# Kernel optimization log

Measured on AMD Instinct MI355X. Metric: run time of the kernel, lower is better.

The kernel has to match this reference:

```python
import jax, jax.numpy as jnp
import numpy as np

N_HEADS = 16
W_INIT_SCALE = 0.02  # GPT-2 style init so activations stay well-conditioned


def setup_inputs() -> dict:
    key = jax.random.key(0)
    k1, k2, k3 = jax.random.split(key, 3)
    B, S, H = 2, 2048, 2048
    return {
        "hidden_states": jax.random.normal(k1, (B, S, H), dtype=jnp.float32),
        "w_attn": jax.random.normal(k2, (H, 3 * H), dtype=jnp.float32) * W_INIT_SCALE,
        "b_attn": jnp.zeros((3 * H,), dtype=jnp.float32),
        "w_proj": jax.random.normal(k3, (H, H), dtype=jnp.float32) * W_INIT_SCALE,
        "b_proj": jnp.zeros((H,), dtype=jnp.float32),
    }


def reference(hidden_states, w_attn, b_attn, w_proj, b_proj):
    B, S, H = hidden_states.shape
    d = H // N_HEADS
    scale = d ** -0.5

    # c_attn: packed QKV projection, then chunk along last dim
    qkv = hidden_states @ w_attn + b_attn  # [B, S, 3H]
    q, k, v = jnp.split(qkv, 3, axis=-1)
    q = q.reshape(B, S, N_HEADS, d)
    k = k.reshape(B, S, N_HEADS, d)
    v = v.reshape(B, S, N_HEADS, d)

    # causal multi-head attention (prompt-phase path of GPTCacheFlowAttention)
    scores = jnp.einsum("bqhd,bkhd->bhqk", q, k) * scale  # [B, H, S, S]
    causal = jnp.tril(jnp.ones((S, S), dtype=bool))
    scores = jnp.where(causal, scores, jnp.finfo(scores.dtype).min)
    probs = jax.nn.softmax(scores, axis=-1)
    attn = jnp.einsum("bhqk,bkhd->bqhd", probs, v).reshape(B, S, H)

    # c_proj output projection
    return attn @ w_proj + b_proj
```

## Files before the change

### kernel.cpp

```cpp
#include <hip/hip_runtime.h>
#include <hip/hip_bf16.h>
#include <stdint.h>

typedef __hip_bfloat16 bf16;
typedef __attribute__((ext_vector_type(4))) float f32x4;
typedef __attribute__((ext_vector_type(8))) short short8;

#define DEVI static __device__ __forceinline__
#define SM_SCALE 0.08838834764831845f

DEVI void gload_lds16(const bf16* g, bf16* l) {
  __builtin_amdgcn_global_load_lds(
      (const __attribute__((address_space(1))) unsigned int*)g,
      (__attribute__((address_space(3))) unsigned int*)l, 16, 0, 0);
}

__global__ __launch_bounds__(256) void cvt_f32_bf16(const float* __restrict__ in,
                                                    bf16* __restrict__ out, int n8) {
  int i = blockIdx.x * blockDim.x + threadIdx.x;
  if (i >= n8) return;
  const float4 a = *(const float4*)(in + (size_t)i * 8);
  const float4 b = *(const float4*)(in + (size_t)i * 8 + 4);
  bf16 t[8];
  t[0] = __float2bfloat16(a.x); t[1] = __float2bfloat16(a.y);
  t[2] = __float2bfloat16(a.z); t[3] = __float2bfloat16(a.w);
  t[4] = __float2bfloat16(b.x); t[5] = __float2bfloat16(b.y);
  t[6] = __float2bfloat16(b.z); t[7] = __float2bfloat16(b.w);
  *(short8*)(out + (size_t)i * 8) = *(const short8*)t;
}

__global__ __launch_bounds__(256) void transpose_cvt(const float* __restrict__ in,
                                                     bf16* __restrict__ out,
                                                     int R, int C, int scale_lt,
                                                     float scale) {
  __shared__ bf16 tile[64][72];
  const int c0 = blockIdx.x * 64, r0 = blockIdx.y * 64;
  const int t = threadIdx.x;
#pragma unroll
  for (int i = 0; i < 4; i++) {
    int idx = (i * 256 + t) * 4;
    int r = idx >> 6, c = idx & 63;
    float4 v = *(const float4*)&in[(size_t)(r0 + r) * C + c0 + c];
    float s0 = (c0 + c + 0 < scale_lt) ? scale : 1.f;
    float s1 = (c0 + c + 1 < scale_lt) ? scale : 1.f;
    float s2 = (c0 + c + 2 < scale_lt) ? scale : 1.f;
    float s3 = (c0 + c + 3 < scale_lt) ? scale : 1.f;
    tile[c + 0][r] = __float2bfloat16(v.x * s0);
    tile[c + 1][r] = __float2bfloat16(v.y * s1);
    tile[c + 2][r] = __float2bfloat16(v.z * s2);
    tile[c + 3][r] = __float2bfloat16(v.w * s3);
  }
  __syncthreads();
#pragma unroll
  for (int i = 0; i < 2; i++) {
    int idx = (i * 256 + t) * 8;
    int c = idx >> 6, r = idx & 63;
    *(short8*)&out[(size_t)(c0 + c) * R + r0 + r] = *(const short8*)&tile[c][r];
  }
}

__global__ __launch_bounds__(256) void build_vt(const bf16* __restrict__ qkv,
                                                bf16* __restrict__ vt) {
  __shared__ bf16 tile[64][72];
  const int bh = blockIdx.z, b = bh >> 4, h = bh & 15;
  const bf16* src = qkv + (size_t)b * 2048 * 6144 + 4096 + (size_t)h * 128;
  bf16* dst = vt + (size_t)bh * 128 * 2048;
  const int s0 = blockIdx.y * 64, d0 = blockIdx.x * 64;
  const int t = threadIdx.x;
#pragma unroll
  for (int i = 0; i < 2; i++) {
    int idx = (i * 256 + t) * 8;
    int r = idx >> 6, c = idx & 63;
    short8 v = *(const short8*)&src[(size_t)(s0 + r) * 6144 + d0 + c];
    bf16* vv = (bf16*)&v;
#pragma unroll
    for (int j = 0; j < 8; j++) tile[c + j][r] = vv[j];
  }
  __syncthreads();
#pragma unroll
  for (int i = 0; i < 2; i++) {
    int idx = (i * 256 + t) * 8;
    int r = idx >> 6, c = idx & 63;
    *(short8*)&dst[(size_t)(d0 + r) * 2048 + s0 + c] = *(const short8*)&tile[r][c];
  }
}

template <int OUT_BF16>
__global__ __launch_bounds__(256, 2) void gemm_bt(const bf16* __restrict__ A,
                                                  const bf16* __restrict__ Bt,
                                                  const float* __restrict__ bias,
                                                  void* __restrict__ C,
                                                  const int M, const int N, const int K,
                                                  const int bias_lt, const float bscale) {
  __shared__ bf16 As[128 * 32];
  __shared__ bf16 Bs[128 * 32];
  const int t = threadIdx.x, lane = t & 63, w = t >> 6;
  const int wr = w >> 1, wc = w & 1;
  const int lrow = lane >> 4, lcol = lane & 15;

  int bid = blockIdx.y * gridDim.x + blockIdx.x;
  const int nwg = gridDim.x * gridDim.y;
  bid = (bid & 7) * (nwg >> 3) + (bid >> 3);
  const int bx = bid % gridDim.x, by = bid / gridDim.x;
  const int m0 = by * 128, n0 = bx * 128;

  f32x4 acc[4][4];
#pragma unroll
  for (int i = 0; i < 4; i++)
#pragma unroll
    for (int j = 0; j < 4; j++) acc[i][j] = (f32x4){0.f, 0.f, 0.f, 0.f};

  for (int k0 = 0; k0 < K; k0 += 32) {
    __syncthreads();
#pragma unroll
    for (int i = 0; i < 2; i++) {
      const int o = i * 256 + t;
      gload_lds16(&A[(size_t)(m0 + (o >> 2)) * K + k0 + ((o & 3) << 3)],
                  &As[(i * 256 + w * 64) * 8]);
      gload_lds16(&Bt[(size_t)(n0 + (o >> 2)) * K + k0 + ((o & 3) << 3)],
                  &Bs[(i * 256 + w * 64) * 8]);
    }
    asm volatile("s_waitcnt vmcnt(0)" ::: "memory");
    __syncthreads();
    short8 af[4], bfr[4];
#pragma unroll
    for (int m = 0; m < 4; m++)
      af[m] = *(const short8*)&As[(wr * 64 + m * 16 + lcol) * 32 + lrow * 8];
#pragma unroll
    for (int n = 0; n < 4; n++)
      bfr[n] = *(const short8*)&Bs[(wc * 64 + n * 16 + lcol) * 32 + lrow * 8];
#pragma unroll
    for (int m = 0; m < 4; m++)
#pragma unroll
      for (int n = 0; n < 4; n++)
        acc[m][n] = __builtin_amdgcn_mfma_f32_16x16x32_bf16(af[m], bfr[n], acc[m][n], 0, 0, 0);
  }

  float bs[4];
#pragma unroll
  for (int n = 0; n < 4; n++) {
    const int col = n0 + wc * 64 + n * 16 + lcol;
    bs[n] = bias[col] * ((col < bias_lt) ? bscale : 1.f);
  }
#pragma unroll
  for (int m = 0; m < 4; m++) {
#pragma unroll
    for (int n = 0; n < 4; n++) {
      const int row = m0 + wr * 64 + m * 16 + lrow * 4;
      const int col = n0 + wc * 64 + n * 16 + lcol;
#pragma unroll
      for (int r = 0; r < 4; r++) {
        float v = acc[m][n][r] + bs[n];
        if (OUT_BF16)
          ((bf16*)C)[(size_t)(row + r) * N + col] = __float2bfloat16(v);
        else
          ((float*)C)[(size_t)(row + r) * N + col] = v;
      }
    }
  }
}

#define FSTEP(q0v, aq, o, mx, ls)                                               \
  {                                                                             \
    f32x4 s[4];                                                                 \
    _Pragma("unroll") for (int n = 0; n < 4; n++) s[n] = (f32x4){0.f, 0.f, 0.f, 0.f}; \
    _Pragma("unroll") for (int n = 0; n < 4; n++) {                             \
      short8 bk[4];                                                             \
      _Pragma("unroll") for (int kc = 0; kc < 4; kc++)                          \
        bk[kc] = *(const short8*)&Kl[n * 16 + lcol][kc * 32 + lrow * 8];        \
      _Pragma("unroll") for (int kc = 0; kc < 4; kc++)                          \
        s[n] = __builtin_amdgcn_mfma_f32_16x16x32_bf16(aq[kc], bk[kc], s[n], 0, 0, 0); \
    }                                                                           \
    if (k0 + 63 > (q0v) + w * 16) {                                             \
      _Pragma("unroll") for (int n = 0; n < 4; n++)                             \
        _Pragma("unroll") for (int r = 0; r < 4; r++) {                         \
          int qg = (q0v) + w * 16 + lrow * 4 + r;                               \
          int kg = k0 + n * 16 + lcol;                                          \
          if (kg > qg) s[n][r] = -1e30f;                                        \
        }                                                                       \
    }                                                                           \
    _Pragma("unroll") for (int r = 0; r < 4; r++) {                             \
      float rm = fmaxf(fmaxf(s[0][r], s[1][r]), fmaxf(s[2][r], s[3][r]));       \
      rm = fmaxf(rm, __shfl_xor(rm, 1));                                        \
      rm = fmaxf(rm, __shfl_xor(rm, 2));                                        \
      rm = fmaxf(rm, __shfl_xor(rm, 4));                                        \
      rm = fmaxf(rm, __shfl_xor(rm, 8));                                        \
      const float mn = fmaxf(mx[r], rm);                                        \
      const float fac = __expf(mx[r] - mn);                                     \
      mx[r] = mn;                                                               \
      float rs = 0.f;                                                           \
      _Pragma("unroll") for (int n = 0; n < 4; n++) {                           \
        float p = __expf(s[n][r] - mn);                                         \
        s[n][r] = p;                                                            \
        rs += p;                                                                \
      }                                                                         \
      rs += __shfl_xor(rs, 1);                                                  \
      rs += __shfl_xor(rs, 2);                                                  \
      rs += __shfl_xor(rs, 4);                                                  \
      rs += __shfl_xor(rs, 8);                                                  \
      ls[r] = ls[r] * fac + rs;                                                 \
      _Pragma("unroll") for (int nd = 0; nd < 8; nd++) o[nd][r] *= fac;         \
    }                                                                           \
    _Pragma("unroll") for (int n = 0; n < 4; n++)                               \
      _Pragma("unroll") for (int r = 0; r < 4; r++)                             \
        Pl[w][lrow * 4 + r][n * 16 + lcol] = __float2bfloat16(s[n][r]);         \
    short8 ap[2];                                                               \
    _Pragma("unroll") for (int kc = 0; kc < 2; kc++)                            \
      ap[kc] = *(const short8*)&Pl[w][lcol][kc * 32 + lrow * 8];                \
    _Pragma("unroll") for (int nd = 0; nd < 8; nd++) {                          \
      short8 bv[2];                                                             \
      _Pragma("unroll") for (int kc = 0; kc < 2; kc++)                          \
        bv[kc] = *(const short8*)&Vl[nd * 16 + lcol][kc * 32 + lrow * 8];       \
      _Pragma("unroll") for (int kc = 0; kc < 2; kc++)                          \
        o[nd] = __builtin_amdgcn_mfma_f32_16x16x32_bf16(ap[kc], bv[kc], o[nd], 0, 0, 0); \
    }                                                                           \
  }

__global__ __launch_bounds__(256, 2) void flash_attn(const bf16* __restrict__ qkv,
                                                     const bf16* __restrict__ vt,
                                                     bf16* __restrict__ attn) {
  constexpr int S = 2048, TH = 6144, HH = 2048, D = 128;
  __shared__ bf16 Kl[64][140];
  __shared__ bf16 Vl[128][76];
  __shared__ bf16 Pl[4][16][76];
  const int t = threadIdx.x, lane = t & 63, w = t >> 6;
  const int lrow = lane >> 4, lcol = lane & 15;

  int id = blockIdx.y * gridDim.x + blockIdx.x;
  id = (id & 7) * 64 + (id >> 3);
  const int i = id & 15, bh = id >> 4;
  const int b = bh >> 4, h = bh & 15;
  const int q0a = i * 64, q0b = (31 - i) * 64;

  const bf16* Qp = qkv + (size_t)b * S * TH + (size_t)h * D;
  const bf16* Kp = Qp + 2048;
  const bf16* Vp = vt + (size_t)bh * D * S;

  short8 aqA[4], aqB[4];
#pragma unroll
  for (int kc = 0; kc < 4; kc++) {
    aqA[kc] = *(const short8*)&Qp[(size_t)(q0a + w * 16 + lcol) * TH + kc * 32 + lrow * 8];
    aqB[kc] = *(const short8*)&Qp[(size_t)(q0b + w * 16 + lcol) * TH + kc * 32 + lrow * 8];
  }

  f32x4 oA[8], oB[8];
  float mxA[4], lsA[4], mxB[4], lsB[4];
#pragma unroll
  for (int nd = 0; nd < 8; nd++) { oA[nd] = (f32x4){0.f,0.f,0.f,0.f}; oB[nd] = (f32x4){0.f,0.f,0.f,0.f}; }
#pragma unroll
  for (int r = 0; r < 4; r++) { mxA[r] = -1e30f; lsA[r] = 0.f; mxB[r] = -1e30f; lsB[r] = 0.f; }

  short8 kreg[4], vreg[4];
#pragma unroll
  for (int i2 = 0; i2 < 4; i2++) {
    int idx = (i2 * 256 + t) * 8;
    int r = idx >> 7, c = idx & 127;
    kreg[i2] = *(const short8*)&Kp[(size_t)r * TH + c];
    int rv = idx >> 6, cv = idx & 63;
    vreg[i2] = *(const short8*)&Vp[(size_t)rv * S + cv];
  }

  const int nkt = 32 - i;
  for (int kt = 0; kt < nkt; ++kt) {
    const int k0 = kt * 64;
    __syncthreads();
#pragma unroll
    for (int i2 = 0; i2 < 4; i2++) {
      int idx = (i2 * 256 + t) * 8;
      int r = idx >> 7, c = idx & 127;
      *(short8*)&Kl[r][c] = kreg[i2];
      int rv = idx >> 6, cv = idx & 63;
      *(short8*)&Vl[rv][cv] = vreg[i2];
    }
    if (kt + 1 < nkt) {
      const int k1 = k0 + 64;
#pragma unroll
      for (int i2 = 0; i2 < 4; i2++) {
        int idx = (i2 * 256 + t) * 8;
        int r = idx >> 7, c = idx & 127;
        kreg[i2] = *(const short8*)&Kp[(size_t)(k1 + r) * TH + c];
        int rv = idx >> 6, cv = idx & 63;
        vreg[i2] = *(const short8*)&Vp[(size_t)rv * S + k1 + cv];
      }
    }
    __syncthreads();
    FSTEP(q0b, aqB, oB, mxB, lsB);
    if (kt <= i) FSTEP(q0a, aqA, oA, mxA, lsA);
  }

#pragma unroll
  for (int nd = 0; nd < 8; nd++)
#pragma unroll
    for (int r = 0; r < 4; r++) {
      attn[(size_t)(b * S + q0a + w * 16 + lrow * 4 + r) * HH + h * D + nd * 16 + lcol] =
          __float2bfloat16(oA[nd][r] / lsA[r]);
      attn[(size_t)(b * S + q0b + w * 16 + lrow * 4 + r) * HH + h * D + nd * 16 + lcol] =
          __float2bfloat16(oB[nd][r] / lsB[r]);
    }
}

extern "C" void kernel_launch(void* const* d_in, const int* in_sizes, int n_in,
                              void* d_out, int out_size, void* d_ws, size_t ws_size,
                              hipStream_t stream) {
  const float* hidden = (const float*)d_in[0];
  const float* w_attn = (const float*)d_in[1];
  const float* b_attn = (const float*)d_in[2];
  const float* w_proj = (const float*)d_in[3];
  const float* b_proj = (const float*)d_in[4];

  char* ws = (char*)d_ws;
  bf16* hb    = (bf16*)(ws);
  bf16* wab_t = (bf16*)(ws + 16777216ull);
  bf16* wpb_t = (bf16*)(ws + 41943040ull);
  bf16* qkv   = (bf16*)(ws + 50331648ull);
  bf16* vt    = (bf16*)(ws + 100663296ull);
  bf16* attn  = (bf16*)(ws + 117440512ull);

  cvt_f32_bf16<<<4096, 256, 0, stream>>>(hidden, hb, 4096 * 2048 / 8);
  transpose_cvt<<<dim3(96, 32), 256, 0, stream>>>(w_attn, wab_t, 2048, 6144, 2048, SM_SCALE);
  transpose_cvt<<<dim3(32, 32), 256, 0, stream>>>(w_proj, wpb_t, 2048, 2048, 0, 1.f);
  gemm_bt<1><<<dim3(48, 32), 256, 0, stream>>>(hb, wab_t, b_attn, (void*)qkv, 4096, 6144, 2048,
                                               2048, SM_SCALE);
  build_vt<<<dim3(2, 32, 32), 256, 0, stream>>>(qkv, vt);
  flash_attn<<<dim3(16, 32), 256, 0, stream>>>(qkv, vt, attn);
  gemm_bt<0><<<dim3(16, 32), 256, 0, stream>>>(attn, wpb_t, b_proj, d_out, 4096, 2048, 2048,
                                               0, 1.f);
}
```

Measured before the change: 423.6 us.

## Use 256x256-tile, 4-stage LDS-pipelined GEMM for QKV projection

Adds a gemm256 kernel with 512 threads that computes 256x256 output tiles. It loads A and B through a 4-deep ring of global_load_lds buffers with XOR-swizzled LDS layout and explicit vmcnt waits, and raises wave priority around the MFMA block. The QKV projection GEMM now uses this kernel instead of the 128x128 gemm_bt, aiming for more operand reuse per byte loaded and better overlap of memory and compute. The cost is 128 KB of LDS and 128 accumulator registers per thread, which limits occupancy, and the grid of 384 blocks may map unevenly onto the CUs.

```diff
diff --git a/kernel.cpp b/kernel.cpp
--- a/kernel.cpp
+++ b/kernel.cpp
@@ -82,6 +82,133 @@
     int idx = (i * 256 + t) * 8;
     int r = idx >> 6, c = idx & 63;
     *(short8*)&dst[(size_t)(d0 + r) * 2048 + s0 + c] = *(const short8*)&tile[r][c];
+  }
+}
+
+#define STAGE(tt)                                                              \
+  {                                                                            \
+    const int sbuf_ = (tt) & 3;                                                \
+    bf16* ab_ = &smem[sbuf_ * 16384 + (w << 9)];                               \
+    bf16* bb_ = &smem[sbuf_ * 16384 + 8192 + (w << 9)];                        \
+    gload_lds16(&A[offA0 + (size_t)(tt) * 32], ab_);                           \
+    gload_lds16(&A[offA1 + (size_t)(tt) * 32], ab_ + 4096);                    \
+    gload_lds16(&Bt[offB0 + (size_t)(tt) * 32], bb_);                          \
+    gload_lds16(&Bt[offB1 + (size_t)(tt) * 32], bb_ + 4096);                   \
+  }
+
+#define GTAIL(tt, NWAIT)                                                       \
+  {                                                                            \
+    asm volatile("s_waitcnt vmcnt(" #NWAIT ")" ::: "memory");                  \
+    asm volatile("s_barrier" ::: "memory");                                    \
+    const int bb = ((tt) & 3) * 16384;                                         \
+    short8 af[8], bfv[4];                                                      \
+    _Pragma("unroll") for (int m = 0; m < 8; m++)                              \
+        af[m] = *(const short8*)&smem[bb + aoe[m]];                            \
+    _Pragma("unroll") for (int n = 0; n < 4; n++)                              \
+        bfv[n] = *(const short8*)&smem[bb + boe[n]];                           \
+    __builtin_amdgcn_s_setprio(1);                                             \
+    _Pragma("unroll") for (int m = 0; m < 8; m++)                              \
+      _Pragma("unroll") for (int n = 0; n < 4; n++)                            \
+        acc[m][n] = __builtin_amdgcn_mfma_f32_16x16x32_bf16(af[m], bfv[n],     \
+                                                            acc[m][n], 0, 0, 0); \
+    __builtin_amdgcn_s_setprio(0);                                             \
+  }
+
+template <int OUT_BF16>
+__global__ __launch_bounds__(512, 2) void gemm256(const bf16* __restrict__ A,
+                                                  const bf16* __restrict__ Bt,
+                                                  const float* __restrict__ bias,
+                                                  void* __restrict__ C,
+                                                  const int M, const int N, const int K,
+                                                  const int bias_lt, const float bscale) {
+  __shared__ bf16 smem[65536];
+  const int t = threadIdx.x, lane = t & 63, w = t >> 6;
+  const int wr = w >> 2, wc = w & 3;
+  const int lrow = lane >> 4, lcol = lane & 15;
+
+  int bid = blockIdx.y * gridDim.x + blockIdx.x;
+  const int nwg = gridDim.x * gridDim.y;
+  bid = (bid & 7) * (nwg >> 3) + (bid >> 3);
+  const int bx = bid % gridDim.x, by = bid / gridDim.x;
+  const int m0 = by * 256, n0 = bx * 256;
+
+  size_t offA0, offA1, offB0, offB1;
+  {
+    int o = (w << 10) + ((lane & 63) << 4);
+    int l0 = o ^ (((o >> 7) & 7) << 4);
+    int o1 = o + 8192;
+    int l1 = o1 ^ (((o1 >> 7) & 7) << 4);
+    offA0 = (size_t)(m0 + (l0 >> 6)) * K + ((l0 & 63) >> 1);
+    offA1 = (size_t)(m0 + (l1 >> 6)) * K + ((l1 & 63) >> 1);
+    offB0 = (size_t)(n0 + (l0 >> 6)) * K + ((l0 & 63) >> 1);
+    offB1 = (size_t)(n0 + (l1 >> 6)) * K + ((l1 & 63) >> 1);
+  }
+  int aoe[8], boe[4];
+#pragma unroll
+  for (int m = 0; m < 8; m++) {
+    int lb = ((wr * 128 + m * 16 + lcol) << 6) + (lrow << 4);
+    lb ^= ((lb >> 7) & 7) << 4;
+    aoe[m] = lb >> 1;
+  }
+#pragma unroll
+  for (int n = 0; n < 4; n++) {
+    int lb = ((wc * 64 + n * 16 + lcol) << 6) + (lrow << 4);
+    lb ^= ((lb >> 7) & 7) << 4;
+    boe[n] = 8192 + (lb >> 1);
+  }
+
+  f32x4 acc[8][4];
+#pragma unroll
+  for (int m = 0; m < 8; m++)
+#pragma unroll
+    for (int n = 0; n < 4; n++) acc[m][n] = (f32x4){0.f, 0.f, 0.f, 0.f};
+
+  const int NT = K >> 5;
+  STAGE(0); STAGE(1); STAGE(2);
+
+  for (int tt = 0; tt < NT - 3; ++tt) {
+    asm volatile("s_waitcnt vmcnt(8)" ::: "memory");
+    asm volatile("s_barrier" ::: "memory");
+    const int bb = (tt & 3) * 16384;
+    short8 af[8], bfv[4];
+#pragma unroll
+    for (int m = 0; m < 8; m++) af[m] = *(const short8*)&smem[bb + aoe[m]];
+#pragma unroll
+    for (int n = 0; n < 4; n++) bfv[n] = *(const short8*)&smem[bb + boe[n]];
+    STAGE(tt + 3);
+    __builtin_amdgcn_s_setprio(1);
+#pragma unroll
+    for (int m = 0; m < 8; m++)
+#pragma unroll
+      for (int n = 0; n < 4; n++)
+        acc[m][n] = __builtin_amdgcn_mfma_f32_16x16x32_bf16(af[m], bfv[n], acc[m][n], 0, 0, 0);
+    __builtin_amdgcn_s_setprio(0);
+  }
+  GTAIL(NT - 3, 8);
+  GTAIL(NT - 2, 4);
+  GTAIL(NT - 1, 0);
+
+  float bs[4];
+#pragma unroll
+  for (int n = 0; n < 4; n++) {
+    const int col = n0 + wc * 64 + n * 16 + lcol;
+    bs[n] = bias[col] * ((col < bias_lt) ? bscale : 1.f);
+  }
+#pragma unroll
+  for (int m = 0; m < 8; m++) {
+#pragma unroll
+    for (int n = 0; n < 4; n++) {
+      const int row = m0 + wr * 128 + m * 16 + lrow * 4;
+      const int col = n0 + wc * 64 + n * 16 + lcol;
+#pragma unroll
+      for (int r = 0; r < 4; r++) {
+        float v = acc[m][n][r] + bs[n];
+        if (OUT_BF16)
+          ((bf16*)C)[(size_t)(row + r) * N + col] = __float2bfloat16(v);
+        else
+          ((float*)C)[(size_t)(row + r) * N + col] = v;
+      }
+    }
   }
 }
 
@@ -319,7 +446,7 @@
   cvt_f32_bf16<<<4096, 256, 0, stream>>>(hidden, hb, 4096 * 2048 / 8);
   transpose_cvt<<<dim3(96, 32), 256, 0, stream>>>(w_attn, wab_t, 2048, 6144, 2048, SM_SCALE);
   transpose_cvt<<<dim3(32, 32), 256, 0, stream>>>(w_proj, wpb_t, 2048, 2048, 0, 1.f);
-  gemm_bt<1><<<dim3(48, 32), 256, 0, stream>>>(hb, wab_t, b_attn, (void*)qkv, 4096, 6144, 2048,
+  gemm256<1><<<dim3(24, 16), 512, 0, stream>>>(hb, wab_t, b_attn, (void*)qkv, 4096, 6144, 2048,
                                                2048, SM_SCALE);
   build_vt<<<dim3(2, 32, 32), 256, 0, stream>>>(qkv, vt);
   flash_attn<<<dim3(16, 32), 256, 0, stream>>>(qkv, vt, attn);
```

Result: faster. 402.8 us (-4.9%).
